# Performance work log

Measured on AMD Instinct MI355X. Metric: run time of the kernel, lower is better.

## Reference

```python
import jax, jax.numpy as jnp
import numpy as np

NUM_EXPERTS = 8
TOP_K = 2
RMS_EPS = 1e-6
SCALING = NUM_EXPERTS / TOP_K


def setup_inputs() -> dict:
    key = jax.random.key(0)
    ks = jax.random.split(key, 6)
    B, S, H, I, E = 4, 2048, 2048, 1024, NUM_EXPERTS
    return {
        "hidden_states": jax.random.normal(ks[0], (B, S, H), dtype=jnp.float32),
        "norm_w": jnp.ones((H,), dtype=jnp.float32),
        "router_w": jax.random.normal(ks[1], (E, H), dtype=jnp.float32) * 0.02,
        "gate_w": jax.random.normal(ks[2], (E, I, H), dtype=jnp.float32) * 0.02,
        "up_w": jax.random.normal(ks[3], (E, I, H), dtype=jnp.float32) * 0.02,
        "down_w": jax.random.normal(ks[4], (E, H, I), dtype=jnp.float32) * 0.02,
    }


def reference(hidden_states, norm_w, router_w, gate_w, up_w, down_w):
    B, S, H = hidden_states.shape
    T = B * S
    flat = hidden_states.reshape(T, H)

    # RMSNorm on router input (fp32 math, as in torch module)
    x32 = flat.astype(jnp.float32)
    var = jnp.mean(x32 * x32, axis=-1, keepdims=True)
    router_input = norm_w * (x32 * jax.lax.rsqrt(var + RMS_EPS))

    # Router: softmax -> top-k -> renormalize
    logits = router_input @ router_w.T                     # [T, E]
    probs = jax.nn.softmax(logits, axis=-1)
    topw, topi = jax.lax.top_k(probs, TOP_K)               # [T, K]
    topw = topw / jnp.sum(topw, axis=-1, keepdims=True)

    # Expert combine: per-token weight for expert e (0 if not selected).
    # Running every token through every expert with weight-0 masking is
    # mathematically identical to the gather/scatter dispatch.
    out = jnp.zeros_like(flat)
    for e in range(NUM_EXPERTS):
        w_e = jnp.sum(jnp.where(topi == e, topw, 0.0), axis=-1)   # [T]
        g = flat @ gate_w[e].T                                    # [T, I]
        u = flat @ up_w[e].T                                      # [T, I]
        o = (jax.nn.silu(g) * u) @ down_w[e].T                    # [T, H]
        out = out + o * w_e[:, None]

    student_output = out.reshape(B, S, H) * SCALING

    # Aux load-balancing loss (training path)
    importance = jnp.sum(probs, axis=0) / T                       # [E]
    load = jnp.sum(topi[..., None] == jnp.arange(NUM_EXPERTS), axis=(0, 1)) / (T * TOP_K)
    aux_loss = jnp.sum(importance * load.astype(jnp.float32)) * NUM_EXPERTS

    return student_output, aux_loss
```

## Files before the change

kernel.cpp:

```cpp
#include <hip/hip_runtime.h>
#include <hip/hip_bf16.h>
#include <cstdint>

#define T_TOKENS 8192
#define H_DIM 2048
#define I_DIM 1024
#define N_EXPERTS 8
#define PAIRS (T_TOKENS * 2)
#define PHASE_TILES 72
#define TOT_TILES (PHASE_TILES*2)
#define TOT_ROWS (TOT_TILES * 128)

using f32x4 = __attribute__((ext_vector_type(4))) float;
using bfv   = __attribute__((ext_vector_type(8))) short;
using u16x8 = __attribute__((ext_vector_type(8))) unsigned short;

typedef __attribute__((address_space(3))) unsigned int lds_u32;
typedef __attribute__((address_space(1))) unsigned int glb_u32;

__device__ __forceinline__ void gll16(const void* g, void* l) {
  __builtin_amdgcn_global_load_lds((const glb_u32*)g, (lds_u32*)l, 16, 0, 0);
}

__device__ inline unsigned short f2bf(float f) {
  unsigned int u = __float_as_uint(f);
  u += 0x7FFFu + ((u >> 16) & 1u);
  return (unsigned short)(u >> 16);
}
__device__ inline float bf2f(unsigned short u) {
  return __uint_as_float((unsigned int)u << 16);
}

__global__ __launch_bounds__(256) void moe_convert_kernel(
    const float* __restrict__ src, unsigned short* __restrict__ dst, int n8) {
  int i = blockIdx.x * 256 + threadIdx.x;
  if (i >= n8) return;
  size_t o = (size_t)i * 8;
  f32x4 a = *reinterpret_cast<const f32x4*>(src + o);
  f32x4 b = *reinterpret_cast<const f32x4*>(src + o + 4);
  u16x8 r = {f2bf(a[0]), f2bf(a[1]), f2bf(a[2]), f2bf(a[3]),
             f2bf(b[0]), f2bf(b[1]), f2bf(b[2]), f2bf(b[3])};
  *reinterpret_cast<u16x8*>(dst + o) = r;
}

__global__ __launch_bounds__(256) void moe_router_kernel(
    const float* __restrict__ X, const float* __restrict__ norm_w,
    const float* __restrict__ rw, float* __restrict__ probs,
    float* __restrict__ topw, int* __restrict__ topi,
    unsigned int* __restrict__ counts, unsigned short* __restrict__ Xb, int writeXb) {
  int t = blockIdx.x;
  int tid = threadIdx.x;
  const float* x = X + (size_t)t * H_DIM;
  int base = tid * 8;
  f32x4 v0 = *reinterpret_cast<const f32x4*>(x + base);
  f32x4 v1 = *reinterpret_cast<const f32x4*>(x + base + 4);
  if (writeXb) {
    u16x8 bx = {f2bf(v0[0]), f2bf(v0[1]), f2bf(v0[2]), f2bf(v0[3]),
                f2bf(v1[0]), f2bf(v1[1]), f2bf(v1[2]), f2bf(v1[3])};
    *reinterpret_cast<u16x8*>(Xb + (size_t)t * H_DIM + base) = bx;
  }
  f32x4 nw0 = *reinterpret_cast<const f32x4*>(norm_w + base);
  f32x4 nw1 = *reinterpret_cast<const f32x4*>(norm_w + base + 4);
  float vals[9];
  vals[0] = v0[0]*v0[0] + v0[1]*v0[1] + v0[2]*v0[2] + v0[3]*v0[3]
          + v1[0]*v1[0] + v1[1]*v1[1] + v1[2]*v1[2] + v1[3]*v1[3];
  f32x4 a0 = v0 * nw0, a1 = v1 * nw1;
#pragma unroll
  for (int e = 0; e < 8; ++e) {
    const float* r = rw + e * H_DIM + base;
    f32x4 r0 = *reinterpret_cast<const f32x4*>(r);
    f32x4 r1 = *reinterpret_cast<const f32x4*>(r + 4);
    f32x4 d = a0 * r0 + a1 * r1;
    vals[e + 1] = d[0] + d[1] + d[2] + d[3];
  }
#pragma unroll
  for (int v = 0; v < 9; ++v) {
    float s = vals[v];
#pragma unroll
    for (int off = 32; off > 0; off >>= 1) s += __shfl_xor(s, off);
    vals[v] = s;
  }
  __shared__ float red[4][9];
  int lane = tid & 63, w = tid >> 6;
  if (lane == 0) {
#pragma unroll
    for (int v = 0; v < 9; ++v) red[w][v] = vals[v];
  }
  __syncthreads();
  if (tid == 0) {
    float tot[9];
#pragma unroll
    for (int v = 0; v < 9; ++v) tot[v] = red[0][v] + red[1][v] + red[2][v] + red[3][v];
    float rs = rsqrtf(tot[0] / (float)H_DIM + 1e-6f);
    float lg[8], mx = -1e30f;
#pragma unroll
    for (int e = 0; e < 8; ++e) { lg[e] = tot[e + 1] * rs; mx = fmaxf(mx, lg[e]); }
    float pe[8], sum = 0.f;
#pragma unroll
    for (int e = 0; e < 8; ++e) { pe[e] = expf(lg[e] - mx); sum += pe[e]; }
    float inv = 1.f / sum;
#pragma unroll
    for (int e = 0; e < 8; ++e) { pe[e] *= inv; probs[t * 8 + e] = pe[e]; }
    int b1 = 0; float p1 = pe[0];
#pragma unroll
    for (int e = 1; e < 8; ++e) if (pe[e] > p1) { p1 = pe[e]; b1 = e; }
    int b2 = -1; float p2 = -1.f;
#pragma unroll
    for (int e = 0; e < 8; ++e) if (e != b1 && pe[e] > p2) { p2 = pe[e]; b2 = e; }
    float wsum = p1 + p2;
    topw[t * 2] = p1 / wsum;
    topw[t * 2 + 1] = p2 / wsum;
    topi[t * 2] = b1;
    topi[t * 2 + 1] = b2;
    atomicAdd(&counts[b1], 1u);
    atomicAdd(&counts[8 + b2], 1u);
  }
}

__global__ __launch_bounds__(256) void moe_importance_kernel(
    const float* __restrict__ probs, float* __restrict__ impSum) {
  int e = blockIdx.x, tid = threadIdx.x;
  float s = 0.f;
  for (int t = tid; t < T_TOKENS; t += 256) s += probs[t * 8 + e];
  __shared__ float red[256];
  red[tid] = s;
  __syncthreads();
  for (int st = 128; st > 0; st >>= 1) {
    if (tid < st) red[tid] += red[tid + st];
    __syncthreads();
  }
  if (tid == 0) impSum[e] = red[0];
}

__global__ void moe_offsets_aux_kernel(const unsigned int* __restrict__ counts,
                                       const float* __restrict__ impSum,
                                       int* __restrict__ tileOff,
                                       float* __restrict__ out_aux) {
  if (threadIdx.x == 0 && blockIdx.x == 0) {
    int acc = 0;
    for (int b = 0; b < 16; ++b) {
      tileOff[b] = acc;
      acc += (int)((counts[b] + 127u) >> 7);
    }
    tileOff[16] = acc;
    float a = 0.f;
    for (int e = 0; e < 8; ++e) {
      float load = (float)(counts[e] + counts[8 + e]) / (float)PAIRS;
      a += (impSum[e] / (float)T_TOKENS) * load;
    }
    out_aux[0] = a * (float)N_EXPERTS;
  }
}

__global__ __launch_bounds__(256) void moe_assign_kernel(
    const int* __restrict__ topi, const int* __restrict__ tileOff,
    unsigned int* __restrict__ cursors, int* __restrict__ row2pair) {
  int p = blockIdx.x * 256 + threadIdx.x;
  if (p >= PAIRS) return;
  int b = topi[p] + 8 * (p & 1);
  unsigned int pos = atomicAdd(&cursors[b], 1u);
  row2pair[tileOff[b] * 128 + (int)pos] = p;
}

template <int PRE>
__global__ __launch_bounds__(256) void moe_stage_a(
    const float* __restrict__ Xf, const unsigned short* __restrict__ Xb,
    const float* __restrict__ gwf, const float* __restrict__ uwf,
    const unsigned short* __restrict__ gwb, const unsigned short* __restrict__ uwb,
    const int* __restrict__ row2pair, const int* __restrict__ tileOff,
    unsigned short* __restrict__ P) {
  __shared__ int sTok[128];
  __shared__ __align__(16) unsigned short sA[128 * 64];
  __shared__ __align__(16) unsigned short sBg[128 * 64];
  __shared__ __align__(16) unsigned short sBu[128 * 64];
  int mt = blockIdx.x;
  if (mt >= tileOff[16]) return;
  int nt = blockIdx.y;
  int b = 0;
#pragma unroll
  for (int k = 1; k < 16; ++k) if (tileOff[k] <= mt) b = k;
  int e = b & 7;
  int row0 = mt * 128, n0 = nt * 128;
  int tid = threadIdx.x;
  if (tid < 128) {
    int pr = row2pair[row0 + tid];
    sTok[tid] = (pr >= 0) ? (pr >> 1) : 0;
  }
  __syncthreads();
  int lane = tid & 63, w = tid >> 6;
  int wm = w >> 1, wn = w & 1;
  int rloc = lane >> 3, cch = lane & 7, swz = cch ^ rloc;
  size_t wb = (size_t)e * ((size_t)I_DIM * H_DIM);

  const unsigned short* srcA[4]; const unsigned short* srcG[4]; const unsigned short* srcU[4];
  const float* fA[4]; const float* fG[4]; const float* fU[4];
#pragma unroll
  for (int i = 0; i < 4; ++i) {
    int s = 4 * w + i;
    int row = s * 8 + rloc;
    int tok = sTok[row];
    int wrow = n0 + row;
    if constexpr (PRE) {
      srcA[i] = Xb + (size_t)tok * H_DIM + swz * 8;
      srcG[i] = gwb + wb + (size_t)wrow * H_DIM + swz * 8;
      srcU[i] = uwb + wb + (size_t)wrow * H_DIM + swz * 8;
    } else {
      fA[i] = Xf + (size_t)tok * H_DIM + cch * 8;
      fG[i] = gwf + wb + (size_t)wrow * H_DIM + cch * 8;
      fU[i] = uwf + wb + (size_t)wrow * H_DIM + cch * 8;
    }
  }
  int wrswz = rloc * 64 + (swz << 3);
  f32x4 accG[4][4] = {};
  f32x4 accU[4][4] = {};
  int lrow = lane & 15, grp = lane >> 4, sw7 = lane & 7;

  for (int kk = 0; kk < H_DIM; kk += 64) {
    if constexpr (PRE) {
#pragma unroll
      for (int i = 0; i < 4; ++i) {
        int lo = (4 * w + i) * 512;
        gll16(srcA[i] + kk, (void*)&sA[lo]);
        gll16(srcG[i] + kk, (void*)&sBg[lo]);
        gll16(srcU[i] + kk, (void*)&sBu[lo]);
      }
      asm volatile("s_waitcnt vmcnt(0)" ::: "memory");
    } else {
#pragma unroll
      for (int i = 0; i < 4; ++i) {
        int o = (4 * w + i) * 512 + wrswz;
        f32x4 x0 = *reinterpret_cast<const f32x4*>(fA[i] + kk);
        f32x4 x1 = *reinterpret_cast<const f32x4*>(fA[i] + kk + 4);
        u16x8 r = {f2bf(x0[0]), f2bf(x0[1]), f2bf(x0[2]), f2bf(x0[3]),
                   f2bf(x1[0]), f2bf(x1[1]), f2bf(x1[2]), f2bf(x1[3])};
        *reinterpret_cast<u16x8*>(&sA[o]) = r;
        x0 = *reinterpret_cast<const f32x4*>(fG[i] + kk);
        x1 = *reinterpret_cast<const f32x4*>(fG[i] + kk + 4);
        u16x8 rg = {f2bf(x0[0]), f2bf(x0[1]), f2bf(x0[2]), f2bf(x0[3]),
                    f2bf(x1[0]), f2bf(x1[1]), f2bf(x1[2]), f2bf(x1[3])};
        *reinterpret_cast<u16x8*>(&sBg[o]) = rg;
        x0 = *reinterpret_cast<const f32x4*>(fU[i] + kk);
        x1 = *reinterpret_cast<const f32x4*>(fU[i] + kk + 4);
        u16x8 ru = {f2bf(x0[0]), f2bf(x0[1]), f2bf(x0[2]), f2bf(x0[3]),
                    f2bf(x1[0]), f2bf(x1[1]), f2bf(x1[2]), f2bf(x1[3])};
        *reinterpret_cast<u16x8*>(&sBu[o]) = ru;
      }
    }
    __syncthreads();
#pragma unroll
    for (int ks = 0; ks < 2; ++ks) {
      int cs = ((ks * 4 + grp) ^ sw7) << 3;
      bfv a[4], bg[4], bu[4];
#pragma unroll
      for (int m = 0; m < 4; ++m)
        a[m] = *reinterpret_cast<const bfv*>(&sA[(wm * 64 + m * 16 + lrow) * 64 + cs]);
#pragma unroll
      for (int n = 0; n < 4; ++n) {
        bg[n] = *reinterpret_cast<const bfv*>(&sBg[(wn * 64 + n * 16 + lrow) * 64 + cs]);
        bu[n] = *reinterpret_cast<const bfv*>(&sBu[(wn * 64 + n * 16 + lrow) * 64 + cs]);
      }
#pragma unroll
      for (int m = 0; m < 4; ++m) {
#pragma unroll
        for (int n = 0; n < 4; ++n) {
          accG[m][n] = __builtin_amdgcn_mfma_f32_16x16x32_bf16(a[m], bg[n], accG[m][n], 0, 0, 0);
          accU[m][n] = __builtin_amdgcn_mfma_f32_16x16x32_bf16(a[m], bu[n], accU[m][n], 0, 0, 0);
        }
      }
    }
    __syncthreads();
  }
  int rbase = grp << 2;
#pragma unroll
  for (int m = 0; m < 4; ++m) {
#pragma unroll
    for (int n = 0; n < 4; ++n) {
#pragma unroll
      for (int j = 0; j < 4; ++j) {
        float g = accG[m][n][j];
        float uu = accU[m][n][j];
        float pv = (g / (1.f + expf(-g))) * uu;
        int rl = wm * 64 + m * 16 + rbase + j;
        int cl = wn * 64 + n * 16 + lrow;
        P[(size_t)(row0 + rl) * I_DIM + n0 + cl] = f2bf(pv);
      }
    }
  }
}

template <int PRE>
__global__ __launch_bounds__(256) void moe_stage_b(
    const unsigned short* __restrict__ Pb,
    const float* __restrict__ dwf, const unsigned short* __restrict__ dwb,
    const int* __restrict__ row2pair, const int* __restrict__ tileOff,
    const float* __restrict__ topw, float* __restrict__ out, int phase) {
  __shared__ int sPair[128];
  __shared__ __align__(16) unsigned short sA[128 * 64];
  __shared__ __align__(16) unsigned short sB[128 * 64];
  int mtEnd = phase ? tileOff[16] : tileOff[8];
  int mt = (phase ? tileOff[8] : 0) + blockIdx.x;
  if (mt >= mtEnd) return;
  int nt = blockIdx.y;
  int b = 0;
#pragma unroll
  for (int k = 1; k < 16; ++k) if (tileOff[k] <= mt) b = k;
  int e = b & 7;
  int row0 = mt * 128, h0 = nt * 128;
  int tid = threadIdx.x;
  if (tid < 128) sPair[tid] = row2pair[row0 + tid];
  __syncthreads();
  int lane = tid & 63, w = tid >> 6;
  int wm = w >> 1, wn = w & 1;
  int rloc = lane >> 3, cch = lane & 7, swz = cch ^ rloc;
  size_t wb = (size_t)e * ((size_t)H_DIM * I_DIM);

  const unsigned short* srcP[4]; const unsigned short* srcD[4]; const float* fD[4];
#pragma unroll
  for (int i = 0; i < 4; ++i) {
    int s = 4 * w + i;
    int row = s * 8 + rloc;
    srcP[i] = Pb + (size_t)(row0 + row) * I_DIM + swz * 8;
    if constexpr (PRE) {
      srcD[i] = dwb + wb + (size_t)(h0 + row) * I_DIM + swz * 8;
    } else {
      fD[i] = dwf + wb + (size_t)(h0 + row) * I_DIM + cch * 8;
    }
  }
  int wrswz = rloc * 64 + (swz << 3);
  f32x4 acc[4][4] = {};
  int lrow = lane & 15, grp = lane >> 4, sw7 = lane & 7;

  for (int kk = 0; kk < I_DIM; kk += 64) {
#pragma unroll
    for (int i = 0; i < 4; ++i) {
      int lo = (4 * w + i) * 512;
      gll16(srcP[i] + kk, (void*)&sA[lo]);
      if constexpr (PRE) gll16(srcD[i] + kk, (void*)&sB[lo]);
    }
    if constexpr (!PRE) {
#pragma unroll
      for (int i = 0; i < 4; ++i) {
        int o = (4 * w + i) * 512 + wrswz;
        f32x4 x0 = *reinterpret_cast<const f32x4*>(fD[i] + kk);
        f32x4 x1 = *reinterpret_cast<const f32x4*>(fD[i] + kk + 4);
        u16x8 r = {f2bf(x0[0]), f2bf(x0[1]), f2bf(x0[2]), f2bf(x0[3]),
                   f2bf(x1[0]), f2bf(x1[1]), f2bf(x1[2]), f2bf(x1[3])};
        *reinterpret_cast<u16x8*>(&sB[o]) = r;
      }
    }
    asm volatile("s_waitcnt vmcnt(0)" ::: "memory");
    __syncthreads();
#pragma unroll
    for (int ks = 0; ks < 2; ++ks) {
      int cs = ((ks * 4 + grp) ^ sw7) << 3;
      bfv a[4], bb[4];
#pragma unroll
      for (int m = 0; m < 4; ++m)
        a[m] = *reinterpret_cast<const bfv*>(&sA[(wm * 64 + m * 16 + lrow) * 64 + cs]);
#pragma unroll
      for (int n = 0; n < 4; ++n)
        bb[n] = *reinterpret_cast<const bfv*>(&sB[(wn * 64 + n * 16 + lrow) * 64 + cs]);
#pragma unroll
      for (int m = 0; m < 4; ++m) {
#pragma unroll
        for (int n = 0; n < 4; ++n)
          acc[m][n] = __builtin_amdgcn_mfma_f32_16x16x32_bf16(a[m], bb[n], acc[m][n], 0, 0, 0);
      }
    }
    __syncthreads();
  }
  int rbase = grp << 2;
#pragma unroll
  for (int m = 0; m < 4; ++m) {
#pragma unroll
    for (int j = 0; j < 4; ++j) {
      int rl = wm * 64 + m * 16 + rbase + j;
      int pr = sPair[rl];
      if (pr < 0) continue;
      float wgt = topw[pr] * 4.f;
      float* orow = out + (size_t)(pr >> 1) * H_DIM + h0 + wn * 64 + lrow;
      if (phase) {
#pragma unroll
        for (int n = 0; n < 4; ++n) orow[n * 16] += wgt * acc[m][n][j];
      } else {
#pragma unroll
        for (int n = 0; n < 4; ++n) orow[n * 16] = wgt * acc[m][n][j];
      }
    }
  }
}

extern "C" void kernel_launch(void* const* d_in, const int* in_sizes, int n_in,
                              void* d_out, int out_size, void* d_ws, size_t ws_size,
                              hipStream_t stream) {
  const float* X = (const float*)d_in[0];
  const float* norm_w = (const float*)d_in[1];
  const float* router_w = (const float*)d_in[2];
  const float* gate_w = (const float*)d_in[3];
  const float* up_w = (const float*)d_in[4];
  const float* down_w = (const float*)d_in[5];
  float* out = (float*)d_out;

  char* ws = (char*)d_ws;
  unsigned short* P = (unsigned short*)(ws);
  float* probs = (float*)(ws + 37748736);
  float* topw = (float*)(ws + 38010880);
  int* topi = (int*)(ws + 38076416);
  int* row2pair = (int*)(ws + 38141952);
  char* ctrl = ws + 38215680;
  unsigned int* counts = (unsigned int*)(ctrl);
  unsigned int* cursors = (unsigned int*)(ctrl + 64);
  float* impSum = (float*)(ctrl + 128);
  int* tileOff = (int*)(ctrl + 192);
  unsigned short* W1 = (unsigned short*)(ws + 38216192);
  unsigned short* W2 = (unsigned short*)(ws + 71770624);
  unsigned short* Xb = (unsigned short*)(ws + 105325056);
  const size_t REQ = 138879488;
  const bool pre = ws_size >= REQ;

  hipMemsetAsync(ctrl, 0, 512, stream);
  hipMemsetAsync(row2pair, 0xFF, (size_t)TOT_ROWS * 4, stream);

  const int N8 = (N_EXPERTS * I_DIM * H_DIM) / 8;
  if (pre) {
    moe_convert_kernel<<<N8 / 256, 256, 0, stream>>>(gate_w, W1, N8);
    moe_convert_kernel<<<N8 / 256, 256, 0, stream>>>(up_w, W2, N8);
  }
  moe_router_kernel<<<T_TOKENS, 256, 0, stream>>>(X, norm_w, router_w, probs, topw, topi,
                                                  counts, Xb, pre ? 1 : 0);
  moe_importance_kernel<<<N_EXPERTS, 256, 0, stream>>>(probs, impSum);
  moe_offsets_aux_kernel<<<1, 64, 0, stream>>>(counts, impSum, tileOff, out + 16777216);
  moe_assign_kernel<<<PAIRS / 256, 256, 0, stream>>>(topi, tileOff, cursors, row2pair);

  if (pre) {
    moe_stage_a<1><<<dim3(TOT_TILES, I_DIM / 128), 256, 0, stream>>>(
        X, Xb, gate_w, up_w, W1, W2, row2pair, tileOff, P);
    moe_convert_kernel<<<N8 / 256, 256, 0, stream>>>(down_w, W1, N8);
    moe_stage_b<1><<<dim3(PHASE_TILES, H_DIM / 128), 256, 0, stream>>>(
        P, down_w, W1, row2pair, tileOff, topw, out, 0);
    moe_stage_b<1><<<dim3(PHASE_TILES, H_DIM / 128), 256, 0, stream>>>(
        P, down_w, W1, row2pair, tileOff, topw, out, 1);
  } else {
    moe_stage_a<0><<<dim3(TOT_TILES, I_DIM / 128), 256, 0, stream>>>(
        X, Xb, gate_w, up_w, W1, W2, row2pair, tileOff, P);
    moe_stage_b<0><<<dim3(PHASE_TILES, H_DIM / 128), 256, 0, stream>>>(
        P, down_w, W1, row2pair, tileOff, topw, out, 0);
    moe_stage_b<0><<<dim3(PHASE_TILES, H_DIM / 128), 256, 0, stream>>>(
        P, down_w, W1, row2pair, tileOff, topw, out, 1);
  }
}
```

Before: 765.9 us.

## Rewrite expert GEMMs as persistent double-buffered 512-thread kernels with work stealing

Both expert GEMM stages become persistent kernels with 512 threads that pull tiles from an atomic work counter. Global-to-LDS loads are double-buffered so the next K-slice is fetched while MFMAs run on the current one. Stage A now reads fp32 activations directly and converts them with packed bf16 conversion instructions, which removes the separate Xb staging buffer. Gate and up weights are interleaved into one B tile, and stage B uses 256-wide output tiles. The fallback path for a small workspace is removed, so the code now assumes enough workspace for the bf16 weight copies.

```diff
diff --git a/kernel.cpp b/kernel.cpp
--- a/kernel.cpp
+++ b/kernel.cpp
@@ -7,13 +7,13 @@
 #define I_DIM 1024
 #define N_EXPERTS 8
 #define PAIRS (T_TOKENS * 2)
-#define PHASE_TILES 72
-#define TOT_TILES (PHASE_TILES*2)
+#define TOT_TILES 144
 #define TOT_ROWS (TOT_TILES * 128)
 
 using f32x4 = __attribute__((ext_vector_type(4))) float;
 using bfv   = __attribute__((ext_vector_type(8))) short;
 using u16x8 = __attribute__((ext_vector_type(8))) unsigned short;
+using u32x4 = __attribute__((ext_vector_type(4))) unsigned int;
 
 typedef __attribute__((address_space(3))) unsigned int lds_u32;
 typedef __attribute__((address_space(1))) unsigned int glb_u32;
@@ -21,14 +21,18 @@
 __device__ __forceinline__ void gll16(const void* g, void* l) {
   __builtin_amdgcn_global_load_lds((const glb_u32*)g, (lds_u32*)l, 16, 0, 0);
 }
+#define SB0() __builtin_amdgcn_sched_barrier(0)
+#define BAR() __builtin_amdgcn_s_barrier()
 
 __device__ inline unsigned short f2bf(float f) {
   unsigned int u = __float_as_uint(f);
   u += 0x7FFFu + ((u >> 16) & 1u);
   return (unsigned short)(u >> 16);
 }
-__device__ inline float bf2f(unsigned short u) {
-  return __uint_as_float((unsigned int)u << 16);
+__device__ __forceinline__ unsigned int pkbf(float lo, float hi) {
+  unsigned int r;
+  asm("v_cvt_pk_bf16_f32 %0, %1, %2" : "=v"(r) : "v"(lo), "v"(hi));
+  return r;
 }
 
 __global__ __launch_bounds__(256) void moe_convert_kernel(
@@ -47,18 +51,13 @@
     const float* __restrict__ X, const float* __restrict__ norm_w,
     const float* __restrict__ rw, float* __restrict__ probs,
     float* __restrict__ topw, int* __restrict__ topi,
-    unsigned int* __restrict__ counts, unsigned short* __restrict__ Xb, int writeXb) {
+    unsigned int* __restrict__ counts) {
   int t = blockIdx.x;
   int tid = threadIdx.x;
   const float* x = X + (size_t)t * H_DIM;
   int base = tid * 8;
   f32x4 v0 = *reinterpret_cast<const f32x4*>(x + base);
   f32x4 v1 = *reinterpret_cast<const f32x4*>(x + base + 4);
-  if (writeXb) {
-    u16x8 bx = {f2bf(v0[0]), f2bf(v0[1]), f2bf(v0[2]), f2bf(v0[3]),
-                f2bf(v1[0]), f2bf(v1[1]), f2bf(v1[2]), f2bf(v1[3])};
-    *reinterpret_cast<u16x8*>(Xb + (size_t)t * H_DIM + base) = bx;
-  }
   f32x4 nw0 = *reinterpret_cast<const f32x4*>(norm_w + base);
   f32x4 nw1 = *reinterpret_cast<const f32x4*>(norm_w + base + 4);
   float vals[9];
@@ -162,229 +161,261 @@
   row2pair[tileOff[b] * 128 + (int)pos] = p;
 }
 
-template <int PRE>
-__global__ __launch_bounds__(256) void moe_stage_a(
-    const float* __restrict__ Xf, const unsigned short* __restrict__ Xb,
-    const float* __restrict__ gwf, const float* __restrict__ uwf,
-    const unsigned short* __restrict__ gwb, const unsigned short* __restrict__ uwb,
+__global__ __launch_bounds__(512, 2) void moe_stage_a(
+    const float* __restrict__ X,
+    const unsigned short* __restrict__ Wg, const unsigned short* __restrict__ Wu,
     const int* __restrict__ row2pair, const int* __restrict__ tileOff,
-    unsigned short* __restrict__ P) {
+    unsigned int* __restrict__ workCtr, unsigned short* __restrict__ P) {
+  __shared__ __align__(16) unsigned short sAB[2][24576];
   __shared__ int sTok[128];
-  __shared__ __align__(16) unsigned short sA[128 * 64];
-  __shared__ __align__(16) unsigned short sBg[128 * 64];
-  __shared__ __align__(16) unsigned short sBu[128 * 64];
-  int mt = blockIdx.x;
-  if (mt >= tileOff[16]) return;
-  int nt = blockIdx.y;
-  int b = 0;
-#pragma unroll
-  for (int k = 1; k < 16; ++k) if (tileOff[k] <= mt) b = k;
-  int e = b & 7;
-  int row0 = mt * 128, n0 = nt * 128;
-  int tid = threadIdx.x;
-  if (tid < 128) {
-    int pr = row2pair[row0 + tid];
-    sTok[tid] = (pr >= 0) ? (pr >> 1) : 0;
-  }
-  __syncthreads();
-  int lane = tid & 63, w = tid >> 6;
-  int wm = w >> 1, wn = w & 1;
-  int rloc = lane >> 3, cch = lane & 7, swz = cch ^ rloc;
-  size_t wb = (size_t)e * ((size_t)I_DIM * H_DIM);
-
-  const unsigned short* srcA[4]; const unsigned short* srcG[4]; const unsigned short* srcU[4];
-  const float* fA[4]; const float* fG[4]; const float* fU[4];
-#pragma unroll
-  for (int i = 0; i < 4; ++i) {
-    int s = 4 * w + i;
-    int row = s * 8 + rloc;
-    int tok = sTok[row];
-    int wrow = n0 + row;
-    if constexpr (PRE) {
-      srcA[i] = Xb + (size_t)tok * H_DIM + swz * 8;
-      srcG[i] = gwb + wb + (size_t)wrow * H_DIM + swz * 8;
-      srcU[i] = uwb + wb + (size_t)wrow * H_DIM + swz * 8;
-    } else {
-      fA[i] = Xf + (size_t)tok * H_DIM + cch * 8;
-      fG[i] = gwf + wb + (size_t)wrow * H_DIM + cch * 8;
-      fU[i] = uwf + wb + (size_t)wrow * H_DIM + cch * 8;
-    }
-  }
-  int wrswz = rloc * 64 + (swz << 3);
-  f32x4 accG[4][4] = {};
-  f32x4 accU[4][4] = {};
-  int lrow = lane & 15, grp = lane >> 4, sw7 = lane & 7;
-
-  for (int kk = 0; kk < H_DIM; kk += 64) {
-    if constexpr (PRE) {
-#pragma unroll
-      for (int i = 0; i < 4; ++i) {
-        int lo = (4 * w + i) * 512;
-        gll16(srcA[i] + kk, (void*)&sA[lo]);
-        gll16(srcG[i] + kk, (void*)&sBg[lo]);
-        gll16(srcU[i] + kk, (void*)&sBu[lo]);
-      }
-      asm volatile("s_waitcnt vmcnt(0)" ::: "memory");
-    } else {
-#pragma unroll
-      for (int i = 0; i < 4; ++i) {
-        int o = (4 * w + i) * 512 + wrswz;
-        f32x4 x0 = *reinterpret_cast<const f32x4*>(fA[i] + kk);
-        f32x4 x1 = *reinterpret_cast<const f32x4*>(fA[i] + kk + 4);
-        u16x8 r = {f2bf(x0[0]), f2bf(x0[1]), f2bf(x0[2]), f2bf(x0[3]),
-                   f2bf(x1[0]), f2bf(x1[1]), f2bf(x1[2]), f2bf(x1[3])};
-        *reinterpret_cast<u16x8*>(&sA[o]) = r;
-        x0 = *reinterpret_cast<const f32x4*>(fG[i] + kk);
-        x1 = *reinterpret_cast<const f32x4*>(fG[i] + kk + 4);
-        u16x8 rg = {f2bf(x0[0]), f2bf(x0[1]), f2bf(x0[2]), f2bf(x0[3]),
-                    f2bf(x1[0]), f2bf(x1[1]), f2bf(x1[2]), f2bf(x1[3])};
-        *reinterpret_cast<u16x8*>(&sBg[o]) = rg;
-        x0 = *reinterpret_cast<const f32x4*>(fU[i] + kk);
-        x1 = *reinterpret_cast<const f32x4*>(fU[i] + kk + 4);
-        u16x8 ru = {f2bf(x0[0]), f2bf(x0[1]), f2bf(x0[2]), f2bf(x0[3]),
-                    f2bf(x1[0]), f2bf(x1[1]), f2bf(x1[2]), f2bf(x1[3])};
-        *reinterpret_cast<u16x8*>(&sBu[o]) = ru;
-      }
-    }
+  __shared__ int sWork;
+  const int tid = threadIdx.x;
+  const int lane = tid & 63, w = tid >> 6;
+  const int wm = w >> 2, wn = w & 3;
+  const int lrow = lane & 15, grp = lane >> 4;
+  const int rloc = lane >> 3, cch = lane & 7;
+  const int swz8 = (cch ^ rloc) * 8;
+  const int ar = tid >> 2, aq = tid & 3;
+  const int ach0 = ((aq * 2) ^ (ar & 7)) * 8;
+  const int ach1 = ((aq * 2 + 1) ^ (ar & 7)) * 8;
+  const int nTiles = tileOff[16];
+  const int nWork = nTiles * 8;
+
+  for (;;) {
+    if (tid == 0) sWork = (int)atomicAdd(workCtr, 1u);
     __syncthreads();
-#pragma unroll
-    for (int ks = 0; ks < 2; ++ks) {
-      int cs = ((ks * 4 + grp) ^ sw7) << 3;
-      bfv a[4], bg[4], bu[4];
-#pragma unroll
-      for (int m = 0; m < 4; ++m)
-        a[m] = *reinterpret_cast<const bfv*>(&sA[(wm * 64 + m * 16 + lrow) * 64 + cs]);
-#pragma unroll
-      for (int n = 0; n < 4; ++n) {
-        bg[n] = *reinterpret_cast<const bfv*>(&sBg[(wn * 64 + n * 16 + lrow) * 64 + cs]);
-        bu[n] = *reinterpret_cast<const bfv*>(&sBu[(wn * 64 + n * 16 + lrow) * 64 + cs]);
-      }
-#pragma unroll
-      for (int m = 0; m < 4; ++m) {
+    const int item = sWork;
+    if (item >= nWork) break;
+    const int mt = item % nTiles;
+    const int nt = item / nTiles;
+    int b = 0;
+#pragma unroll
+    for (int k = 1; k < 16; ++k) if (tileOff[k] <= mt) b = k;
+    const int e = b & 7;
+    const int row0 = mt * 128, n0 = nt * 128;
+    if (tid < 128) {
+      int pr = row2pair[row0 + tid];
+      sTok[tid] = (pr >= 0) ? (pr >> 1) : 0;
+    }
+    __syncthreads();
+
+    const float* aSrc = X + (size_t)sTok[ar] * H_DIM + aq * 16;
+    const unsigned short* bSrc[4];
+    const size_t wbase = (size_t)e * ((size_t)I_DIM * H_DIM);
+#pragma unroll
+    for (int i = 0; i < 4; ++i) {
+      int s = 4 * w + i;
+      int col = n0 + (s >> 3) * 32 + (s & 3) * 8 + rloc;
+      const unsigned short* basep = (s & 4) ? Wu : Wg;
+      bSrc[i] = basep + wbase + (size_t)col * H_DIM + swz8;
+    }
+    const int bDst = 8192 + 4 * w * 512 + lane * 8;
+
+    f32x4 acc[4][4] = {};
+
+    {
+      f32x4 a0 = *reinterpret_cast<const f32x4*>(aSrc);
+      f32x4 a1 = *reinterpret_cast<const f32x4*>(aSrc + 4);
+      f32x4 a2 = *reinterpret_cast<const f32x4*>(aSrc + 8);
+      f32x4 a3 = *reinterpret_cast<const f32x4*>(aSrc + 12);
+      SB0();
+#pragma unroll
+      for (int i = 0; i < 4; ++i)
+        gll16(bSrc[i], (void*)&sAB[0][bDst + i * 512]);
+      SB0();
+      u32x4 q0 = {pkbf(a0[0], a0[1]), pkbf(a0[2], a0[3]), pkbf(a1[0], a1[1]), pkbf(a1[2], a1[3])};
+      u32x4 q1 = {pkbf(a2[0], a2[1]), pkbf(a2[2], a2[3]), pkbf(a3[0], a3[1]), pkbf(a3[2], a3[3])};
+      *reinterpret_cast<u32x4*>(&sAB[0][ar * 64 + ach0]) = q0;
+      *reinterpret_cast<u32x4*>(&sAB[0][ar * 64 + ach1]) = q1;
+      asm volatile("s_waitcnt lgkmcnt(0)" ::: "memory");
+      SB0();
+      BAR();
+      SB0();
+    }
+
+    int cur = 0;
+#pragma unroll 1
+    for (int kk = 0; kk < 32; ++kk) {
+      f32x4 a0, a1, a2, a3;
+      if (kk < 31) {
+        const float* ap = aSrc + (kk + 1) * 64;
+        a0 = *reinterpret_cast<const f32x4*>(ap);
+        a1 = *reinterpret_cast<const f32x4*>(ap + 4);
+        a2 = *reinterpret_cast<const f32x4*>(ap + 8);
+        a3 = *reinterpret_cast<const f32x4*>(ap + 12);
+        SB0();
+#pragma unroll
+        for (int i = 0; i < 4; ++i)
+          gll16(bSrc[i] + (kk + 1) * 64, (void*)&sAB[cur ^ 1][bDst + i * 512]);
+        SB0();
+        asm volatile("s_waitcnt vmcnt(8)" ::: "memory");
+      } else {
+        asm volatile("s_waitcnt vmcnt(0)" ::: "memory");
+      }
+      SB0();
+      BAR();
+      SB0();
+#pragma unroll
+      for (int ks = 0; ks < 2; ++ks) {
+        bfv af[4], bf[4];
+        const int co = ((ks * 4 + grp) ^ cch) << 3;
+#pragma unroll
+        for (int m = 0; m < 4; ++m) {
+          int r = wm * 64 + m * 16 + lrow;
+          af[m] = *reinterpret_cast<const bfv*>(&sAB[cur][r * 64 + co]);
+        }
 #pragma unroll
         for (int n = 0; n < 4; ++n) {
-          accG[m][n] = __builtin_amdgcn_mfma_f32_16x16x32_bf16(a[m], bg[n], accG[m][n], 0, 0, 0);
-          accU[m][n] = __builtin_amdgcn_mfma_f32_16x16x32_bf16(a[m], bu[n], accU[m][n], 0, 0, 0);
-        }
-      }
-    }
+          int R = wn * 64 + n * 16 + lrow;
+          bf[n] = *reinterpret_cast<const bfv*>(&sAB[cur][8192 + R * 64 + co]);
+        }
+#pragma unroll
+        for (int m = 0; m < 4; ++m)
+#pragma unroll
+          for (int n = 0; n < 4; ++n)
+            acc[m][n] = __builtin_amdgcn_mfma_f32_16x16x32_bf16(af[m], bf[n], acc[m][n], 0, 0, 0);
+      }
+      if (kk < 31) {
+        u32x4 q0 = {pkbf(a0[0], a0[1]), pkbf(a0[2], a0[3]), pkbf(a1[0], a1[1]), pkbf(a1[2], a1[3])};
+        u32x4 q1 = {pkbf(a2[0], a2[1]), pkbf(a2[2], a2[3]), pkbf(a3[0], a3[1]), pkbf(a3[2], a3[3])};
+        *reinterpret_cast<u32x4*>(&sAB[cur ^ 1][ar * 64 + ach0]) = q0;
+        *reinterpret_cast<u32x4*>(&sAB[cur ^ 1][ar * 64 + ach1]) = q1;
+        asm volatile("s_waitcnt lgkmcnt(0)" ::: "memory");
+      }
+      SB0();
+      BAR();
+      cur ^= 1;
+    }
+
+    const int rb = grp * 4;
+#pragma unroll
+    for (int m = 0; m < 4; ++m) {
+#pragma unroll
+      for (int n = 0; n < 2; ++n) {
+#pragma unroll
+        for (int j = 0; j < 4; ++j) {
+          float g = acc[m][n][j];
+          float uu = acc[m][n + 2][j];
+          float pv = (g / (1.f + expf(-g))) * uu;
+          int rl = wm * 64 + m * 16 + rb + j;
+          int cl = n0 + wn * 32 + n * 16 + lrow;
+          P[(size_t)(row0 + rl) * I_DIM + cl] = f2bf(pv);
+        }
+      }
+    }
+  }
+}
+
+__global__ __launch_bounds__(512, 2) void moe_stage_b(
+    const unsigned short* __restrict__ Pb, const unsigned short* __restrict__ Wd,
+    const int* __restrict__ row2pair, const int* __restrict__ tileOff,
+    const float* __restrict__ topw, unsigned int* __restrict__ workCtr,
+    float* __restrict__ out, int phase) {
+  __shared__ __align__(16) unsigned short sAB[2][24576];
+  __shared__ int sPair[128];
+  __shared__ int sWork;
+  const int tid = threadIdx.x;
+  const int lane = tid & 63, w = tid >> 6;
+  const int wm = w >> 2, wn = w & 3;
+  const int lrow = lane & 15, grp = lane >> 4;
+  const int rloc = lane >> 3, cch = lane & 7;
+  const int swz8 = (cch ^ rloc) * 8;
+  const int t0 = phase ? tileOff[8] : 0;
+  const int t1 = phase ? tileOff[16] : tileOff[8];
+  const int nTiles = t1 - t0;
+  const int nWork = nTiles * 8;
+  const int ldsOff = 6 * w * 512 + lane * 8;
+
+  for (;;) {
+    if (tid == 0) sWork = (int)atomicAdd(workCtr, 1u);
     __syncthreads();
-  }
-  int rbase = grp << 2;
-#pragma unroll
-  for (int m = 0; m < 4; ++m) {
-#pragma unroll
-    for (int n = 0; n < 4; ++n) {
+    const int item = sWork;
+    if (item >= nWork) break;
+    const int mt = t0 + item % nTiles;
+    const int nt = item / nTiles;
+    int b = 0;
+#pragma unroll
+    for (int k = 1; k < 16; ++k) if (tileOff[k] <= mt) b = k;
+    const int e = b & 7;
+    const int row0 = mt * 128, h0 = nt * 256;
+    if (tid < 128) sPair[tid] = row2pair[row0 + tid];
+    __syncthreads();
+
+    const unsigned short* src[6];
+#pragma unroll
+    for (int i = 0; i < 6; ++i) {
+      int s = 6 * w + i;
+      if (s < 16) {
+        src[i] = Pb + (size_t)(row0 + s * 8 + rloc) * I_DIM + swz8;
+      } else {
+        int sb = s - 16;
+        src[i] = Wd + (size_t)e * ((size_t)H_DIM * I_DIM) +
+                 (size_t)(h0 + sb * 8 + rloc) * I_DIM + swz8;
+      }
+    }
+    f32x4 acc[4][4] = {};
+
+#pragma unroll
+    for (int i = 0; i < 6; ++i)
+      gll16(src[i], (void*)&sAB[0][ldsOff + i * 512]);
+
+    int cur = 0;
+#pragma unroll 1
+    for (int kk = 0; kk < 16; ++kk) {
+      if (kk < 15) {
+#pragma unroll
+        for (int i = 0; i < 6; ++i)
+          gll16(src[i] + (kk + 1) * 64, (void*)&sAB[cur ^ 1][ldsOff + i * 512]);
+        SB0();
+        asm volatile("s_waitcnt vmcnt(6)" ::: "memory");
+      } else {
+        asm volatile("s_waitcnt vmcnt(0)" ::: "memory");
+      }
+      SB0();
+      BAR();
+      SB0();
+#pragma unroll
+      for (int ks = 0; ks < 2; ++ks) {
+        bfv af[4], bf[4];
+        const int co = ((ks * 4 + grp) ^ cch) << 3;
+#pragma unroll
+        for (int m = 0; m < 4; ++m) {
+          int r = wm * 64 + m * 16 + lrow;
+          af[m] = *reinterpret_cast<const bfv*>(&sAB[cur][r * 64 + co]);
+        }
+#pragma unroll
+        for (int n = 0; n < 4; ++n) {
+          int R = wn * 64 + n * 16 + lrow;
+          bf[n] = *reinterpret_cast<const bfv*>(&sAB[cur][8192 + R * 64 + co]);
+        }
+#pragma unroll
+        for (int m = 0; m < 4; ++m)
+#pragma unroll
+          for (int n = 0; n < 4; ++n)
+            acc[m][n] = __builtin_amdgcn_mfma_f32_16x16x32_bf16(af[m], bf[n], acc[m][n], 0, 0, 0);
+      }
+      SB0();
+      BAR();
+      cur ^= 1;
+    }
+
+    const int rb = grp * 4;
+#pragma unroll
+    for (int m = 0; m < 4; ++m) {
 #pragma unroll
       for (int j = 0; j < 4; ++j) {
-        float g = accG[m][n][j];
-        float uu = accU[m][n][j];
-        float pv = (g / (1.f + expf(-g))) * uu;
-        int rl = wm * 64 + m * 16 + rbase + j;
-        int cl = wn * 64 + n * 16 + lrow;
-        P[(size_t)(row0 + rl) * I_DIM + n0 + cl] = f2bf(pv);
-      }
-    }
-  }
-}
-
-template <int PRE>
-__global__ __launch_bounds__(256) void moe_stage_b(
-    const unsigned short* __restrict__ Pb,
-    const float* __restrict__ dwf, const unsigned short* __restrict__ dwb,
-    const int* __restrict__ row2pair, const int* __restrict__ tileOff,
-    const float* __restrict__ topw, float* __restrict__ out, int phase) {
-  __shared__ int sPair[128];
-  __shared__ __align__(16) unsigned short sA[128 * 64];
-  __shared__ __align__(16) unsigned short sB[128 * 64];
-  int mtEnd = phase ? tileOff[16] : tileOff[8];
-  int mt = (phase ? tileOff[8] : 0) + blockIdx.x;
-  if (mt >= mtEnd) return;
-  int nt = blockIdx.y;
-  int b = 0;
-#pragma unroll
-  for (int k = 1; k < 16; ++k) if (tileOff[k] <= mt) b = k;
-  int e = b & 7;
-  int row0 = mt * 128, h0 = nt * 128;
-  int tid = threadIdx.x;
-  if (tid < 128) sPair[tid] = row2pair[row0 + tid];
-  __syncthreads();
-  int lane = tid & 63, w = tid >> 6;
-  int wm = w >> 1, wn = w & 1;
-  int rloc = lane >> 3, cch = lane & 7, swz = cch ^ rloc;
-  size_t wb = (size_t)e * ((size_t)H_DIM * I_DIM);
-
-  const unsigned short* srcP[4]; const unsigned short* srcD[4]; const float* fD[4];
-#pragma unroll
-  for (int i = 0; i < 4; ++i) {
-    int s = 4 * w + i;
-    int row = s * 8 + rloc;
-    srcP[i] = Pb + (size_t)(row0 + row) * I_DIM + swz * 8;
-    if constexpr (PRE) {
-      srcD[i] = dwb + wb + (size_t)(h0 + row) * I_DIM + swz * 8;
-    } else {
-      fD[i] = dwf + wb + (size_t)(h0 + row) * I_DIM + cch * 8;
-    }
-  }
-  int wrswz = rloc * 64 + (swz << 3);
-  f32x4 acc[4][4] = {};
-  int lrow = lane & 15, grp = lane >> 4, sw7 = lane & 7;
-
-  for (int kk = 0; kk < I_DIM; kk += 64) {
-#pragma unroll
-    for (int i = 0; i < 4; ++i) {
-      int lo = (4 * w + i) * 512;
-      gll16(srcP[i] + kk, (void*)&sA[lo]);
-      if constexpr (PRE) gll16(srcD[i] + kk, (void*)&sB[lo]);
-    }
-    if constexpr (!PRE) {
-#pragma unroll
-      for (int i = 0; i < 4; ++i) {
-        int o = (4 * w + i) * 512 + wrswz;
-        f32x4 x0 = *reinterpret_cast<const f32x4*>(fD[i] + kk);
-        f32x4 x1 = *reinterpret_cast<const f32x4*>(fD[i] + kk + 4);
-        u16x8 r = {f2bf(x0[0]), f2bf(x0[1]), f2bf(x0[2]), f2bf(x0[3]),
-                   f2bf(x1[0]), f2bf(x1[1]), f2bf(x1[2]), f2bf(x1[3])};
-        *reinterpret_cast<u16x8*>(&sB[o]) = r;
-      }
-    }
-    asm volatile("s_waitcnt vmcnt(0)" ::: "memory");
-    __syncthreads();
-#pragma unroll
-    for (int ks = 0; ks < 2; ++ks) {
-      int cs = ((ks * 4 + grp) ^ sw7) << 3;
-      bfv a[4], bb[4];
-#pragma unroll
-      for (int m = 0; m < 4; ++m)
-        a[m] = *reinterpret_cast<const bfv*>(&sA[(wm * 64 + m * 16 + lrow) * 64 + cs]);
-#pragma unroll
-      for (int n = 0; n < 4; ++n)
-        bb[n] = *reinterpret_cast<const bfv*>(&sB[(wn * 64 + n * 16 + lrow) * 64 + cs]);
-#pragma unroll
-      for (int m = 0; m < 4; ++m) {
-#pragma unroll
-        for (int n = 0; n < 4; ++n)
-          acc[m][n] = __builtin_amdgcn_mfma_f32_16x16x32_bf16(a[m], bb[n], acc[m][n], 0, 0, 0);
-      }
-    }
-    __syncthreads();
-  }
-  int rbase = grp << 2;
-#pragma unroll
-  for (int m = 0; m < 4; ++m) {
-#pragma unroll
-    for (int j = 0; j < 4; ++j) {
-      int rl = wm * 64 + m * 16 + rbase + j;
-      int pr = sPair[rl];
-      if (pr < 0) continue;
-      float wgt = topw[pr] * 4.f;
-      float* orow = out + (size_t)(pr >> 1) * H_DIM + h0 + wn * 64 + lrow;
-      if (phase) {
-#pragma unroll
-        for (int n = 0; n < 4; ++n) orow[n * 16] += wgt * acc[m][n][j];
-      } else {
-#pragma unroll
-        for (int n = 0; n < 4; ++n) orow[n * 16] = wgt * acc[m][n][j];
+        int rl = wm * 64 + m * 16 + rb + j;
+        int pr = sPair[rl];
+        if (pr < 0) continue;
+        float wgt = topw[pr] * 4.f;
+        float* orow = out + (size_t)(pr >> 1) * H_DIM + h0 + wn * 64 + lrow;
+        if (phase) {
+#pragma unroll
+          for (int n = 0; n < 4; ++n) orow[n * 16] += wgt * acc[m][n][j];
+        } else {
+#pragma unroll
+          for (int n = 0; n < 4; ++n) orow[n * 16] = wgt * acc[m][n][j];
+        }
       }
     }
   }
@@ -412,40 +443,26 @@
   unsigned int* cursors = (unsigned int*)(ctrl + 64);
   float* impSum = (float*)(ctrl + 128);
   int* tileOff = (int*)(ctrl + 192);
+  unsigned int* wcA = (unsigned int*)(ctrl + 384);
+  unsigned int* wcB0 = (unsigned int*)(ctrl + 388);
+  unsigned int* wcB1 = (unsigned int*)(ctrl + 392);
   unsigned short* W1 = (unsigned short*)(ws + 38216192);
   unsigned short* W2 = (unsigned short*)(ws + 71770624);
-  unsigned short* Xb = (unsigned short*)(ws + 105325056);
-  const size_t REQ = 138879488;
-  const bool pre = ws_size >= REQ;
 
   hipMemsetAsync(ctrl, 0, 512, stream);
   hipMemsetAsync(row2pair, 0xFF, (size_t)TOT_ROWS * 4, stream);
 
   const int N8 = (N_EXPERTS * I_DIM * H_DIM) / 8;
-  if (pre) {
-    moe_convert_kernel<<<N8 / 256, 256, 0, stream>>>(gate_w, W1, N8);
-    moe_convert_kernel<<<N8 / 256, 256, 0, stream>>>(up_w, W2, N8);
-  }
-  moe_router_kernel<<<T_TOKENS, 256, 0, stream>>>(X, norm_w, router_w, probs, topw, topi,
-                                                  counts, Xb, pre ? 1 : 0);
+  moe_convert_kernel<<<N8 / 256, 256, 0, stream>>>(gate_w, W1, N8);
+  moe_convert_kernel<<<N8 / 256, 256, 0, stream>>>(up_w, W2, N8);
+
+  moe_router_kernel<<<T_TOKENS, 256, 0, stream>>>(X, norm_w, router_w, probs, topw, topi, counts);
   moe_importance_kernel<<<N_EXPERTS, 256, 0, stream>>>(probs, impSum);
   moe_offsets_aux_kernel<<<1, 64, 0, stream>>>(counts, impSum, tileOff, out + 16777216);
   moe_assign_kernel<<<PAIRS / 256, 256, 0, stream>>>(topi, tileOff, cursors, row2pair);
 
-  if (pre) {
-    moe_stage_a<1><<<dim3(TOT_TILES, I_DIM / 128), 256, 0, stream>>>(
-        X, Xb, gate_w, up_w, W1, W2, row2pair, tileOff, P);
-    moe_convert_kernel<<<N8 / 256, 256, 0, stream>>>(down_w, W1, N8);
-    moe_stage_b<1><<<dim3(PHASE_TILES, H_DIM / 128), 256, 0, stream>>>(
-        P, down_w, W1, row2pair, tileOff, topw, out, 0);
-    moe_stage_b<1><<<dim3(PHASE_TILES, H_DIM / 128), 256, 0, stream>>>(
-        P, down_w, W1, row2pair, tileOff, topw, out, 1);
-  } else {
-    moe_stage_a<0><<<dim3(TOT_TILES, I_DIM / 128), 256, 0, stream>>>(
-        X, Xb, gate_w, up_w, W1, W2, row2pair, tileOff, P);
-    moe_stage_b<0><<<dim3(PHASE_TILES, H_DIM / 128), 256, 0, stream>>>(
-        P, down_w, W1, row2pair, tileOff, topw, out, 0);
-    moe_stage_b<0><<<dim3(PHASE_TILES, H_DIM / 128), 256, 0, stream>>>(
-        P, down_w, W1, row2pair, tileOff, topw, out, 1);
-  }
-}
+  moe_stage_a<<<256, 512, 0, stream>>>(X, W1, W2, row2pair, tileOff, wcA, P);
+  moe_convert_kernel<<<N8 / 256, 256, 0, stream>>>(down_w, W1, N8);
+  moe_stage_b<<<256, 512, 0, stream>>>(P, W1, row2pair, tileOff, topw, wcB0, out, 0);
+  moe_stage_b<<<256, 512, 0, stream>>>(P, W1, row2pair, tileOff, topw, wcB1, out, 1);
+}
```

New measurement: 769.6 us (median of 2 runs). About the same (+0.5%).
